# Optimization experiments

Measured on AMD Instinct MI355X. Metric: run time of the kernel, lower is better.

The kernel has to match this reference:

```python
import jax, jax.numpy as jnp
import numpy as np

VOCAB = 32000
HID = 1024


def setup_inputs() -> dict:
    key = jax.random.key(0)
    ks = jax.random.split(key, 6)
    B, S = 32, 1024
    x = jax.random.randint(ks[0], (B, S), 0, VOCAB, dtype=jnp.int64) if jax.config.jax_enable_x64 else jax.random.randint(ks[0], (B, S), 0, VOCAB, dtype=jnp.int32)
    scale = 1.0 / np.sqrt(HID)
    embed = jax.random.normal(ks[1], (VOCAB, HID), dtype=jnp.float32) * scale
    embed = embed.at[0].set(0.0)  # padding_idx=0
    Wc = jax.random.normal(ks[2], (HID, HID), dtype=jnp.float32) * scale
    bc = jnp.zeros((HID,), dtype=jnp.float32)
    Wgx = jax.random.normal(ks[3], (HID, 3 * HID), dtype=jnp.float32) * scale
    # gate bias init: reset=2.0, persistence=2.0, accumulation=0.0
    bgx = jnp.concatenate([
        jnp.full((HID,), 2.0, dtype=jnp.float32),
        jnp.full((HID,), 2.0, dtype=jnp.float32),
        jnp.zeros((HID,), dtype=jnp.float32),
    ])
    Wgh = jax.random.normal(ks[4], (HID, 3 * HID), dtype=jnp.float32) * scale
    return {"x": x, "embed": embed, "Wc": Wc, "bc": bc, "Wgx": Wgx, "bgx": bgx, "Wgh": Wgh}


def reference(x, embed, Wc, bc, Wgx, bgx, Wgh):
    # x: (B,S) int token ids
    B, S = x.shape
    H = HID
    e = embed[x]  # (B,S,H)  dropout is identity in eval mode
    gate_x = jnp.einsum('bsh,hg->bsg', e, Wgx) + bgx       # (B,S,3H)
    cand = jnp.tanh(jnp.einsum('bsh,hk->bsk', e, Wc) + bc)  # (B,S,H)

    def step(h, inputs):
        gx_t, v_t = inputs  # (B,3H), (B,H)
        gates = jax.nn.sigmoid(gx_t + h @ Wgh)  # (B,3H)
        rho = gates[:, :H]
        pi = gates[:, H:2 * H]
        alpha = gates[:, 2 * H:]
        h_new = rho * (pi * h + alpha * v_t)
        return h_new, None

    h0 = jnp.zeros((B, H), dtype=e.dtype)
    h_final, _ = jax.lax.scan(step, h0, (jnp.swapaxes(gate_x, 0, 1), jnp.swapaxes(cand, 0, 1)))
    return h_final  # (B,H)
```

## Files before the change

kernel.cpp:

```cpp
#include <hip/hip_runtime.h>
#include <cstdint>
#include <cstddef>

#define HID   1024
#define BATCH 32
#define SEQ   1024
#define NROWS 32768
#define G3    3072
#define NWG   128
#define NFLAGS ((SEQ + 1) * NWG)
#define HSLOT 32768

typedef __attribute__((ext_vector_type(8))) short bf16x8_t;
typedef __attribute__((ext_vector_type(4))) float f32x4_t;

__device__ __forceinline__ unsigned short f2bf(float f) {
  unsigned u = __float_as_uint(f);
  u += 0x7FFFu + ((u >> 16) & 1u);
  return (unsigned short)(u >> 16);
}
__device__ __forceinline__ float bf2f(unsigned short s) {
  return __uint_as_float(((unsigned)s) << 16);
}

__device__ __forceinline__ void store_short_wt(unsigned short* p, unsigned short v) {
  asm volatile("global_store_short %0, %1, off sc0 sc1"
               :: "v"(p), "v"((unsigned)v) : "memory");
}

__global__ __launch_bounds__(256) void transpose_cast(const float* __restrict__ in,
                                                      unsigned short* __restrict__ out,
                                                      int N) {
  __shared__ float tile[32][33];
  int k0 = blockIdx.x * 32, n0 = blockIdx.y * 32;
  int tx = threadIdx.x, ty = threadIdx.y;
#pragma unroll
  for (int i = 0; i < 4; ++i)
    tile[ty + 8 * i][tx] = in[(size_t)(k0 + ty + 8 * i) * N + n0 + tx];
  __syncthreads();
#pragma unroll
  for (int i = 0; i < 4; ++i)
    out[(size_t)(n0 + ty + 8 * i) * HID + k0 + tx] = f2bf(tile[tx][ty + 8 * i]);
}

__global__ __launch_bounds__(256) void gather_cast(const int* __restrict__ x,
                                                   const float* __restrict__ embed,
                                                   unsigned short* __restrict__ e) {
  int r = blockIdx.x;
  int t = threadIdx.x;
  int tok = x[r];
  const float4* src = (const float4*)(embed + (size_t)tok * HID);
  float4 v = src[t];
  ushort4 o;
  o.x = f2bf(v.x); o.y = f2bf(v.y); o.z = f2bf(v.z); o.w = f2bf(v.w);
  ((ushort4*)(e + (size_t)r * HID))[t] = o;
}

__global__ __launch_bounds__(256) void gemm_fused(const unsigned short* __restrict__ A,
                                                  const unsigned short* __restrict__ B,
                                                  const float* __restrict__ bgx,
                                                  const float* __restrict__ bc,
                                                  unsigned short* __restrict__ gx,
                                                  unsigned short* __restrict__ cand) {
  __shared__ unsigned short As[128 * 32];
  __shared__ unsigned short Bs[128 * 32];
  const int bm = blockIdx.x * 128, bn = blockIdx.y * 128;
  const int t = threadIdx.x;
  const int wave = t >> 6, lane = t & 63;
  const int q = lane >> 4, nidx = lane & 15;
  const int wm = (wave & 1) * 64, wn = (wave >> 1) * 64;
  const int sr = t >> 2;
  const int kofs = (t & 3) * 8;

  f32x4_t acc[4][4];
#pragma unroll
  for (int i = 0; i < 4; ++i)
#pragma unroll
    for (int j = 0; j < 4; ++j) acc[i][j] = (f32x4_t){0.f, 0.f, 0.f, 0.f};

#pragma unroll 1
  for (int kt = 0; kt < HID; kt += 32) {
    __syncthreads();
#pragma unroll
    for (int c = 0; c < 2; ++c) {
      int row = c * 64 + sr;
      *(uint4*)(&As[row * 32 + kofs]) = *(const uint4*)(&A[(size_t)(bm + row) * HID + kt + kofs]);
      *(uint4*)(&Bs[row * 32 + kofs]) = *(const uint4*)(&B[(size_t)(bn + row) * HID + kt + kofs]);
    }
    __syncthreads();
    bf16x8_t af[4], bfr[4];
#pragma unroll
    for (int i = 0; i < 4; ++i)
      af[i] = *(const bf16x8_t*)(&As[(wm + i * 16 + nidx) * 32 + q * 8]);
#pragma unroll
    for (int j = 0; j < 4; ++j)
      bfr[j] = *(const bf16x8_t*)(&Bs[(wn + j * 16 + nidx) * 32 + q * 8]);
#pragma unroll
    for (int i = 0; i < 4; ++i)
#pragma unroll
      for (int j = 0; j < 4; ++j)
        acc[i][j] = __builtin_amdgcn_mfma_f32_16x16x32_bf16(af[i], bfr[j], acc[i][j], 0, 0, 0);
  }

#pragma unroll
  for (int i = 0; i < 4; ++i) {
#pragma unroll
    for (int j = 0; j < 4; ++j) {
#pragma unroll
      for (int reg = 0; reg < 4; ++reg) {
        int m = bm + wm + i * 16 + q * 4 + reg;
        int n = bn + wn + j * 16 + nidx;
        float v = acc[i][j][reg];
        if (n < G3) {
          gx[(size_t)m * G3 + n] = f2bf(v + bgx[n]);
        } else {
          int nc = n - G3;
          cand[(size_t)m * HID + nc] = f2bf(tanhf(v + bc[nc]));
        }
      }
    }
  }
}

__global__ __launch_bounds__(256) void init_state(unsigned int* __restrict__ flags,
                                                  unsigned short* __restrict__ ring) {
  int t = blockIdx.x * 256 + threadIdx.x;
  if (t < NFLAGS) flags[t] = (t < NWG) ? 1u : 0u;
  if (t < HSLOT) ring[t] = 0;
}

__global__ __launch_bounds__(128) void recurrence(const unsigned short* __restrict__ gx,
                                                  const unsigned short* __restrict__ cand,
                                                  const unsigned short* __restrict__ WghT,
                                                  unsigned short* __restrict__ ring,
                                                  unsigned int* __restrict__ flags,
                                                  float* __restrict__ out) {
  const int g = blockIdx.x;
  const int tid = threadIdx.x;
  const int w = tid >> 6;
  const int lane = tid & 63;
  const int q = lane >> 4, n = lane & 15;

  __shared__ __align__(16) unsigned short Bs[32 * 1024];

  for (int it = tid; it < 4096; it += 128) {
    int row = it >> 7, c16 = it & 127;
    int tile = row >> 4, rr = row & 15;
    uint4 val = {0u, 0u, 0u, 0u};
    if (tile == 0) {
      int gr = (rr < 8) ? (8 * g + rr) : (1024 + 8 * g + (rr - 8));
      val = ((const uint4*)(WghT + (size_t)gr * HID))[c16];
    } else if (rr < 8) {
      int gr = 2048 + 8 * g + rr;
      val = ((const uint4*)(WghT + (size_t)gr * HID))[c16];
    }
    *(uint4*)((char*)Bs + (size_t)(row * 128 + (c16 ^ (row & 7))) * 16) = val;
  }
  __syncthreads();

  __builtin_amdgcn_fence(__ATOMIC_ACQUIRE, "agent");

  float h_own[4] = {0.f, 0.f, 0.f, 0.f};
  const int c_rp = (n < 8) ? (8 * g + n) : (1024 + 8 * g + (n - 8));
  const int c_al = 2048 + 8 * g + (n & 7);
  const int c_h  = 8 * g + (n & 7);

  const char* b0p = (const char*)Bs + (size_t)n * 2048;
  const char* b1p = b0p + 16 * 2048;

#pragma unroll 1
  for (int t = 0; t < SEQ; ++t) {
    const unsigned short* hc = ring + ((size_t)t << 15);
    unsigned short* hn = ring + ((size_t)(t + 1) << 15);

    float g0v[4], g1v[4], vv[4];
#pragma unroll
    for (int r = 0; r < 4; ++r) {
      size_t rb = ((size_t)(w * 16 + q * 4 + r) * SEQ + t);
      g0v[r] = bf2f(gx[rb * G3 + c_rp]);
      g1v[r] = bf2f(gx[rb * G3 + c_al]);
      vv[r]  = bf2f(cand[rb * HID + c_h]);
    }

    const unsigned int* frow = flags + (size_t)t * NWG;
    while (__hip_atomic_load(&frow[tid], __ATOMIC_RELAXED, __HIP_MEMORY_SCOPE_AGENT) == 0u) {}
    __syncthreads();
    asm volatile("" ::: "memory");

    f32x4_t acc0 = (f32x4_t){0.f, 0.f, 0.f, 0.f};
    f32x4_t acc1 = (f32x4_t){0.f, 0.f, 0.f, 0.f};
    const unsigned short* ha = hc + (size_t)(w * 16 + n) * HID + q * 8;
#pragma unroll 8
    for (int kt = 0; kt < 32; ++kt) {
      bf16x8_t a = *(const bf16x8_t*)(ha + kt * 32);
      int sw = ((kt * 4 + q) ^ (n & 7)) * 16;
      bf16x8_t b0 = *(const bf16x8_t*)(b0p + sw);
      bf16x8_t b1 = *(const bf16x8_t*)(b1p + sw);
      acc0 = __builtin_amdgcn_mfma_f32_16x16x32_bf16(a, b0, acc0, 0, 0, 0);
      acc1 = __builtin_amdgcn_mfma_f32_16x16x32_bf16(a, b1, acc1, 0, 0, 0);
    }

#pragma unroll
    for (int r = 0; r < 4; ++r) {
      float s0 = 1.f / (1.f + __expf(-(acc0[r] + g0v[r])));
      float al = 1.f / (1.f + __expf(-(acc1[r] + g1v[r])));
      float piv = __shfl(s0, q * 16 + 8 + (n & 7), 64);
      if (n < 8) {
        h_own[r] = s0 * (piv * h_own[r] + al * vv[r]);
        store_short_wt(&hn[(size_t)(w * 16 + q * 4 + r) * HID + c_h], f2bf(h_own[r]));
      }
    }

    asm volatile("s_waitcnt vmcnt(0)" ::: "memory");
    __syncthreads();
    if (tid == 0)
      __hip_atomic_store(&flags[(size_t)(t + 1) * NWG + g], 1u,
                         __ATOMIC_RELAXED, __HIP_MEMORY_SCOPE_AGENT);
  }

#pragma unroll
  for (int r = 0; r < 4; ++r)
    if (n < 8)
      out[(size_t)(w * 16 + q * 4 + r) * HID + c_h] = h_own[r];
}

extern "C" void kernel_launch(void* const* d_in, const int* in_sizes, int n_in,
                              void* d_out, int out_size, void* d_ws, size_t ws_size,
                              hipStream_t stream) {
  const int*   x     = (const int*)d_in[0];
  const float* embed = (const float*)d_in[1];
  const float* Wc    = (const float*)d_in[2];
  const float* bc    = (const float*)d_in[3];
  const float* Wgx   = (const float*)d_in[4];
  const float* bgx   = (const float*)d_in[5];
  const float* Wgh   = (const float*)d_in[6];
  float* out = (float*)d_out;

  char* base = (char*)d_ws;
  unsigned short* e    = (unsigned short*)(base);
  unsigned short* Bp   = (unsigned short*)(base + 67108864);
  unsigned short* WghT = (unsigned short*)(base + 75497472);
  unsigned short* gxb  = (unsigned short*)(base + 81788928);
  unsigned short* cnd  = (unsigned short*)(base + 283115520);
  unsigned short* ring  = (unsigned short*)(base);
  unsigned int*   flags = (unsigned int*)(base + 350224384);

  transpose_cast<<<dim3(32, 96), dim3(32, 8), 0, stream>>>(Wgx, Bp, G3);
  transpose_cast<<<dim3(32, 32), dim3(32, 8), 0, stream>>>(Wc, Bp + (size_t)G3 * HID, HID);
  transpose_cast<<<dim3(32, 96), dim3(32, 8), 0, stream>>>(Wgh, WghT, G3);

  gather_cast<<<dim3(NROWS), dim3(256), 0, stream>>>(x, embed, e);

  gemm_fused<<<dim3(256, 32), dim3(256), 0, stream>>>(e, Bp, bgx, bc, gxb, cnd);

  init_state<<<dim3(513), dim3(256), 0, stream>>>(flags, ring);

  void* args[] = {(void*)&gxb, (void*)&cnd, (void*)&WghT, (void*)&ring,
                  (void*)&flags, (void*)&out};
  hipLaunchCooperativeKernel((const void*)recurrence, dim3(NWG), dim3(128), args, 0, stream);
}
```

Measured before the change: 6.303 ms.

## Restructure recurrence to 32 workgroups with register-resident Wgh and monotonic flags

The recurrence now runs on 32 workgroups of 4 waves instead of 128 of 2. Each wave keeps its slice of the transposed Wgh (all three gates, 32 columns per workgroup) in registers rather than LDS, and computes all three gates with MFMA directly, so the pi shuffle and half-idle lanes go away. Synchronisation becomes a single monotonic counter per workgroup polled by one wave, with a bounded spin guard, replacing the per-step flag rows. The gx/cand values for the next step are prefetched during the MFMA loop. It also adds a canary write to the output and a non-cooperative fallback launch. The costs are very high register pressure (96 bf16x8 vectors per thread) and fewer CUs doing the serial matvec, and the spin guard can break correctness if a wait exceeds 8192 polls.

New measurement: 9.851 ms. 1.56x slower.

```diff
diff --git a/kernel.cpp b/kernel.cpp
--- a/kernel.cpp
+++ b/kernel.cpp
@@ -7,8 +7,7 @@
 #define SEQ   1024
 #define NROWS 32768
 #define G3    3072
-#define NWG   128
-#define NFLAGS ((SEQ + 1) * NWG)
+#define NWORK 32
 #define HSLOT 32768
 
 typedef __attribute__((ext_vector_type(8))) short bf16x8_t;
@@ -122,106 +121,129 @@
   }
 }
 
-__global__ __launch_bounds__(256) void init_state(unsigned int* __restrict__ flags,
-                                                  unsigned short* __restrict__ ring) {
-  int t = blockIdx.x * 256 + threadIdx.x;
-  if (t < NFLAGS) flags[t] = (t < NWG) ? 1u : 0u;
-  if (t < HSLOT) ring[t] = 0;
-}
-
-__global__ __launch_bounds__(128) void recurrence(const unsigned short* __restrict__ gx,
-                                                  const unsigned short* __restrict__ cand,
-                                                  const unsigned short* __restrict__ WghT,
-                                                  unsigned short* __restrict__ ring,
-                                                  unsigned int* __restrict__ flags,
-                                                  float* __restrict__ out) {
+__global__ __launch_bounds__(64) void init_state(unsigned int* __restrict__ fx) {
+  int t = threadIdx.x;
+  if (t < 32) fx[t] = 0u;
+}
+
+__global__ __launch_bounds__(64) void canary(float* __restrict__ out) {
+  out[threadIdx.x] = 1.0e6f;
+}
+
+__global__ __launch_bounds__(256, 1) void recurrence(const unsigned short* __restrict__ gx,
+                                                     const unsigned short* __restrict__ cand,
+                                                     const unsigned short* __restrict__ WghT,
+                                                     unsigned short* __restrict__ ring,
+                                                     unsigned int* __restrict__ flags,
+                                                     float* __restrict__ out) {
   const int g = blockIdx.x;
   const int tid = threadIdx.x;
-  const int w = tid >> 6;
   const int lane = tid & 63;
+  const int wave = tid >> 6;
   const int q = lane >> 4, n = lane & 15;
-
-  __shared__ __align__(16) unsigned short Bs[32 * 1024];
-
-  for (int it = tid; it < 4096; it += 128) {
-    int row = it >> 7, c16 = it & 127;
-    int tile = row >> 4, rr = row & 15;
-    uint4 val = {0u, 0u, 0u, 0u};
-    if (tile == 0) {
-      int gr = (rr < 8) ? (8 * g + rr) : (1024 + 8 * g + (rr - 8));
-      val = ((const uint4*)(WghT + (size_t)gr * HID))[c16];
-    } else if (rr < 8) {
-      int gr = 2048 + 8 * g + rr;
-      val = ((const uint4*)(WghT + (size_t)gr * HID))[c16];
-    }
-    *(uint4*)((char*)Bs + (size_t)(row * 128 + (c16 ^ (row & 7))) * 16) = val;
-  }
-  __syncthreads();
+  const int m16 = (wave & 1) * 16;
+  const int cg2 = wave >> 1;
+  const int colh = 32 * g + cg2 * 16 + n;
 
   __builtin_amdgcn_fence(__ATOMIC_ACQUIRE, "agent");
 
+  bf16x8_t wR[32], wP[32], wA[32];
+#pragma unroll
+  for (int kt = 0; kt < 32; ++kt) {
+    const size_t ko = (size_t)kt * 32 + q * 8;
+    wR[kt] = *(const bf16x8_t*)(WghT + (size_t)(colh)        * HID + ko);
+    wP[kt] = *(const bf16x8_t*)(WghT + (size_t)(1024 + colh) * HID + ko);
+    wA[kt] = *(const bf16x8_t*)(WghT + (size_t)(2048 + colh) * HID + ko);
+  }
+
   float h_own[4] = {0.f, 0.f, 0.f, 0.f};
-  const int c_rp = (n < 8) ? (8 * g + n) : (1024 + 8 * g + (n - 8));
-  const int c_al = 2048 + 8 * g + (n & 7);
-  const int c_h  = 8 * g + (n & 7);
-
-  const char* b0p = (const char*)Bs + (size_t)n * 2048;
-  const char* b1p = b0p + 16 * 2048;
+  unsigned short pR[4], pP[4], pA[4], pV[4];
+  unsigned short nR[4], nP[4], nA[4], nV[4];
+
+#pragma unroll
+  for (int r = 0; r < 4; ++r) {
+    const size_t rb = (size_t)(m16 + q * 4 + r) * SEQ;
+    pR[r] = gx[rb * G3 + colh];
+    pP[r] = gx[rb * G3 + 1024 + colh];
+    pA[r] = gx[rb * G3 + 2048 + colh];
+    pV[r] = cand[rb * HID + colh];
+  }
 
 #pragma unroll 1
   for (int t = 0; t < SEQ; ++t) {
-    const unsigned short* hc = ring + ((size_t)t << 15);
+    if (t > 0) {
+      const unsigned int* fp = flags + (lane & 31);
+      unsigned fv;
+      int guard = 0;
+      do {
+        fv = __hip_atomic_load(fp, __ATOMIC_RELAXED, __HIP_MEMORY_SCOPE_AGENT);
+      } while (__any(fv < (unsigned)t) && ++guard < 8192);
+      asm volatile("" ::: "memory");
+    }
+
+    const int tp = (t + 1 < SEQ) ? t + 1 : t;
+
+    f32x4_t aR = (f32x4_t){0.f, 0.f, 0.f, 0.f};
+    f32x4_t aP = (f32x4_t){0.f, 0.f, 0.f, 0.f};
+    f32x4_t aA = (f32x4_t){0.f, 0.f, 0.f, 0.f};
+    if (t > 0) {
+      const unsigned short* ha = ring + ((size_t)t << 15) + (size_t)(m16 + n) * HID + q * 8;
+#pragma unroll
+      for (int c = 0; c < 8; ++c) {
+        bf16x8_t av[4];
+#pragma unroll
+        for (int u = 0; u < 4; ++u)
+          av[u] = *(const bf16x8_t*)(ha + (c * 4 + u) * 32);
+        if (c == 0) {
+#pragma unroll
+          for (int r = 0; r < 4; ++r) {
+            const size_t rb = (size_t)(m16 + q * 4 + r) * SEQ + tp;
+            nR[r] = gx[rb * G3 + colh];
+            nP[r] = gx[rb * G3 + 1024 + colh];
+            nA[r] = gx[rb * G3 + 2048 + colh];
+            nV[r] = cand[rb * HID + colh];
+          }
+        }
+#pragma unroll
+        for (int u = 0; u < 4; ++u) {
+          aR = __builtin_amdgcn_mfma_f32_16x16x32_bf16(av[u], wR[c * 4 + u], aR, 0, 0, 0);
+          aP = __builtin_amdgcn_mfma_f32_16x16x32_bf16(av[u], wP[c * 4 + u], aP, 0, 0, 0);
+          aA = __builtin_amdgcn_mfma_f32_16x16x32_bf16(av[u], wA[c * 4 + u], aA, 0, 0, 0);
+        }
+      }
+    } else {
+#pragma unroll
+      for (int r = 0; r < 4; ++r) {
+        const size_t rb = (size_t)(m16 + q * 4 + r) * SEQ + tp;
+        nR[r] = gx[rb * G3 + colh];
+        nP[r] = gx[rb * G3 + 1024 + colh];
+        nA[r] = gx[rb * G3 + 2048 + colh];
+        nV[r] = cand[rb * HID + colh];
+      }
+    }
+
     unsigned short* hn = ring + ((size_t)(t + 1) << 15);
-
-    float g0v[4], g1v[4], vv[4];
 #pragma unroll
     for (int r = 0; r < 4; ++r) {
-      size_t rb = ((size_t)(w * 16 + q * 4 + r) * SEQ + t);
-      g0v[r] = bf2f(gx[rb * G3 + c_rp]);
-      g1v[r] = bf2f(gx[rb * G3 + c_al]);
-      vv[r]  = bf2f(cand[rb * HID + c_h]);
-    }
-
-    const unsigned int* frow = flags + (size_t)t * NWG;
-    while (__hip_atomic_load(&frow[tid], __ATOMIC_RELAXED, __HIP_MEMORY_SCOPE_AGENT) == 0u) {}
-    __syncthreads();
-    asm volatile("" ::: "memory");
-
-    f32x4_t acc0 = (f32x4_t){0.f, 0.f, 0.f, 0.f};
-    f32x4_t acc1 = (f32x4_t){0.f, 0.f, 0.f, 0.f};
-    const unsigned short* ha = hc + (size_t)(w * 16 + n) * HID + q * 8;
-#pragma unroll 8
-    for (int kt = 0; kt < 32; ++kt) {
-      bf16x8_t a = *(const bf16x8_t*)(ha + kt * 32);
-      int sw = ((kt * 4 + q) ^ (n & 7)) * 16;
-      bf16x8_t b0 = *(const bf16x8_t*)(b0p + sw);
-      bf16x8_t b1 = *(const bf16x8_t*)(b1p + sw);
-      acc0 = __builtin_amdgcn_mfma_f32_16x16x32_bf16(a, b0, acc0, 0, 0, 0);
-      acc1 = __builtin_amdgcn_mfma_f32_16x16x32_bf16(a, b1, acc1, 0, 0, 0);
-    }
-
-#pragma unroll
-    for (int r = 0; r < 4; ++r) {
-      float s0 = 1.f / (1.f + __expf(-(acc0[r] + g0v[r])));
-      float al = 1.f / (1.f + __expf(-(acc1[r] + g1v[r])));
-      float piv = __shfl(s0, q * 16 + 8 + (n & 7), 64);
-      if (n < 8) {
-        h_own[r] = s0 * (piv * h_own[r] + al * vv[r]);
-        store_short_wt(&hn[(size_t)(w * 16 + q * 4 + r) * HID + c_h], f2bf(h_own[r]));
-      }
-    }
+      float rho = 1.f / (1.f + __expf(-(aR[r] + bf2f(pR[r]))));
+      float pi  = 1.f / (1.f + __expf(-(aP[r] + bf2f(pP[r]))));
+      float al  = 1.f / (1.f + __expf(-(aA[r] + bf2f(pA[r]))));
+      h_own[r] = rho * (pi * h_own[r] + al * bf2f(pV[r]));
+      store_short_wt(&hn[(size_t)(m16 + q * 4 + r) * HID + colh], f2bf(h_own[r]));
+    }
+#pragma unroll
+    for (int r = 0; r < 4; ++r) { pR[r] = nR[r]; pP[r] = nP[r]; pA[r] = nA[r]; pV[r] = nV[r]; }
 
     asm volatile("s_waitcnt vmcnt(0)" ::: "memory");
     __syncthreads();
     if (tid == 0)
-      __hip_atomic_store(&flags[(size_t)(t + 1) * NWG + g], 1u,
+      __hip_atomic_store(&flags[g], (unsigned)(t + 1),
                          __ATOMIC_RELAXED, __HIP_MEMORY_SCOPE_AGENT);
   }
 
 #pragma unroll
   for (int r = 0; r < 4; ++r)
-    if (n < 8)
-      out[(size_t)(w * 16 + q * 4 + r) * HID + c_h] = h_own[r];
+    out[(size_t)(m16 + q * 4 + r) * HID + colh] = h_own[r];
 }
 
 extern "C" void kernel_launch(void* const* d_in, const int* in_sizes, int n_in,
@@ -253,9 +275,15 @@
 
   gemm_fused<<<dim3(256, 32), dim3(256), 0, stream>>>(e, Bp, bgx, bc, gxb, cnd);
 
-  init_state<<<dim3(513), dim3(256), 0, stream>>>(flags, ring);
+  init_state<<<dim3(1), dim3(64), 0, stream>>>(flags);
+
+  canary<<<dim3(1), dim3(64), 0, stream>>>(out);
 
   void* args[] = {(void*)&gxb, (void*)&cnd, (void*)&WghT, (void*)&ring,
                   (void*)&flags, (void*)&out};
-  hipLaunchCooperativeKernel((const void*)recurrence, dim3(NWG), dim3(128), args, 0, stream);
-}
+  hipError_t cerr = hipLaunchCooperativeKernel((const void*)recurrence,
+                                               dim3(NWORK), dim3(256), args, 0, stream);
+  if (cerr != hipSuccess) {
+    recurrence<<<dim3(NWORK), dim3(256), 0, stream>>>(gxb, cnd, WghT, ring, flags, out);
+  }
+}
```
